# Optimization experiments

Hardware: AMD Instinct MI355X
Metric: run time of the kernel (lower is better)

The kernel has to match this reference:

```python
import jax, jax.numpy as jnp
import numpy as np

N_NODES = 50000
N_EDGES = 800000
D = 256            # node_feat_size
D_EDGE = 16        # edge_feat_size (unused in forward math, as in the original)
G_FEAT = 200       # graph_feat_size
N_TASKS = 1
N_GRAPHS = 512


def _p(key, shape):
    return jax.random.normal(key, shape, dtype=jnp.float32) * 0.05


def setup_inputs() -> dict:
    key = jax.random.key(0)
    ks = jax.random.split(key, 24)
    inp = {
        'node_feats_1': jax.random.normal(ks[0], (N_NODES, D), dtype=jnp.float32),
        'edge_feats_1': jax.random.normal(ks[1], (N_EDGES, D_EDGE), dtype=jnp.float32),
        'node_feats_2': jax.random.normal(ks[2], (N_NODES, D), dtype=jnp.float32),
        'edge_feats_2': jax.random.normal(ks[3], (N_EDGES, D_EDGE), dtype=jnp.float32),
        'src_1': jax.random.randint(ks[4], (N_EDGES,), 0, N_NODES, dtype=jnp.int32),
        'dst_1': jax.random.randint(ks[5], (N_EDGES,), 0, N_NODES, dtype=jnp.int32),
        'graph_ids_1': jnp.sort(jax.random.randint(ks[6], (N_NODES,), 0, N_GRAPHS, dtype=jnp.int32)),
        'src_2': jax.random.randint(ks[7], (N_EDGES,), 0, N_NODES, dtype=jnp.int32),
        'dst_2': jax.random.randint(ks[8], (N_EDGES,), 0, N_NODES, dtype=jnp.int32),
        'graph_ids_2': jnp.sort(jax.random.randint(ks[9], (N_NODES,), 0, N_GRAPHS, dtype=jnp.int32)),
        # GCN layer 1 params (GraphConv weight/bias + residual Linear)
        'W1': _p(ks[10], (D, D)), 'b1': jnp.zeros((D,), jnp.float32),
        'Wr1': _p(ks[11], (D, D)), 'br1': jnp.zeros((D,), jnp.float32),
        # GCN layer 2 params
        'W2': _p(ks[12], (D, D)), 'b2': jnp.zeros((D,), jnp.float32),
        'Wr2': _p(ks[13], (D, D)), 'br2': jnp.zeros((D,), jnp.float32),
        # Readout 1 MLP
        'Ri1': _p(ks[14], (D, D)), 'rbi1': jnp.zeros((D,), jnp.float32),
        'Ro1': _p(ks[15], (D, G_FEAT)), 'rbo1': jnp.zeros((G_FEAT,), jnp.float32),
        # Readout 2 MLP
        'Ri2': _p(ks[16], (D, D)), 'rbi2': jnp.zeros((D,), jnp.float32),
        'Ro2': _p(ks[17], (D, G_FEAT)), 'rbo2': jnp.zeros((G_FEAT,), jnp.float32),
        # Predictor
        'Wp': _p(ks[18], (G_FEAT, N_TASKS)), 'bp': jnp.zeros((N_TASKS,), jnp.float32),
    }
    return inp


def _gcn_layer(h, src, dst, W, b, Wr, br):
    # DGL GraphConv, norm='none': project, aggregate (sum src->dst), bias, relu
    hW = h @ W                                             # [N, D]
    agg = jax.ops.segment_sum(jnp.take(hW, src, axis=0), dst, num_segments=N_NODES)
    conv = jax.nn.relu(agg + b)
    # residual branch: activation(Linear(h))
    res = jax.nn.relu(h @ Wr + br)
    return conv + res                                      # dropout=0, no batchnorm


def _readout(h, graph_ids, Wi, bi, Wo, bo):
    # MLPNodeReadout: Linear -> relu -> Linear, then sum over nodes per graph
    h = jax.nn.relu(h @ Wi + bi)
    h = h @ Wo + bo                                        # [N, G_FEAT]
    return jax.ops.segment_sum(h, graph_ids, num_segments=N_GRAPHS)


def reference(node_feats_1, edge_feats_1, node_feats_2, edge_feats_2,
              src_1, dst_1, graph_ids_1, src_2, dst_2, graph_ids_2,
              W1, b1, Wr1, br1, W2, b2, Wr2, br2,
              Ri1, rbi1, Ro1, rbo1, Ri2, rbi2, Ro2, rbo2, Wp, bp):
    h1 = _gcn_layer(node_feats_1, src_1, dst_1, W1, b1, Wr1, br1)
    g1 = _readout(h1, graph_ids_1, Ri1, rbi1, Ro1, rbo1)
    h2 = _gcn_layer(node_feats_2, src_2, dst_2, W2, b2, Wr2, br2)
    g2 = _readout(h2, graph_ids_2, Ri2, rbi2, Ro2, rbo2)
    g = g1 + g2                                            # [G, G_FEAT]
    return (g @ Wp + bp).reshape(-1)                       # [G * n_tasks]
```

## Files before the change

### kernel.cpp

```cpp
#include <hip/hip_runtime.h>

#define NN 50000
#define NE 800000
#define DD 256
#define GFEAT 200
#define NG 512

typedef __bf16 bf16;
typedef bf16 bf16x4 __attribute__((ext_vector_type(4)));
typedef bf16 bf16x8 __attribute__((ext_vector_type(8)));
typedef float f32x4 __attribute__((ext_vector_type(4)));

__device__ __forceinline__ void gl_lds16(const bf16* g, bf16* l) {
    __builtin_amdgcn_global_load_lds(
        (const __attribute__((address_space(1))) uint32_t*)(g),
        (__attribute__((address_space(3))) uint32_t*)(l), 16, 0, 0);
}

__device__ __forceinline__ bf16x8 frag_ld64(const bf16* s, int R, int C) {
    return *(const bf16x8*)&s[R * 64 + ((C ^ ((R >> 1) & 7)) << 3)];
}

#define EPI_STRIDE 136

__global__ __launch_bounds__(256) void conv_x2_kernel(const float* __restrict__ in0,
                                                      const float* __restrict__ in1,
                                                      bf16* __restrict__ out0,
                                                      bf16* __restrict__ out1, int n4) {
    const float* in = blockIdx.y ? in1 : in0;
    bf16* out = blockIdx.y ? out1 : out0;
    int i = blockIdx.x * 256 + threadIdx.x;
    if (i < n4) {
        float4 v = ((const float4*)in)[i];
        bf16x4 o;
        o[0] = (bf16)v.x; o[1] = (bf16)v.y; o[2] = (bf16)v.z; o[3] = (bf16)v.w;
        ((bf16x4*)out)[i] = o;
    }
}

__global__ __launch_bounds__(256) void conv_w8_kernel(
    const float* __restrict__ w0, const float* __restrict__ w1,
    const float* __restrict__ w2, const float* __restrict__ w3,
    const float* __restrict__ w4, const float* __restrict__ w5,
    const float* __restrict__ w6, const float* __restrict__ w7,
    bf16* __restrict__ out_base) {
    const float* ws[8] = {w0, w1, w2, w3, w4, w5, w6, w7};
    const int Ns[8] = {DD, DD, DD, GFEAT, DD, DD, DD, GFEAT};
    int m = blockIdx.y;
    const float* in = ws[m];
    int N = Ns[m];
    int idx = blockIdx.x * 256 + threadIdx.x;
    int n = idx >> 8, k = idx & 255;
    float v = (n < N) ? in[k * N + n] : 0.f;
    out_base[(size_t)m * 65536 + idx] = (bf16)v;
}

__global__ __launch_bounds__(256) void zero_g_kernel(float* __restrict__ G0,
                                                     float* __restrict__ G1) {
    float* G = blockIdx.y ? G1 : G0;
    int i = blockIdx.x * 256 + threadIdx.x;
    if (i < NG * GFEAT) G[i] = 0.f;
}

#define NBKT   128
#define NPB    391
#define NCHUNK 256
#define CE     ((NE + NCHUNK - 1) / NCHUNK)

__global__ __launch_bounds__(256) void csr_coarse_hist_kernel(
    const int* __restrict__ d0, const int* __restrict__ d1,
    int* __restrict__ cnt0, int* __restrict__ cnt1) {
    const int blk = blockIdx.x, t = threadIdx.x;
    const int* dst = blockIdx.y ? d1 : d0;
    int* cnt = blockIdx.y ? cnt1 : cnt0;
    __shared__ int hist[NBKT];
    if (t < NBKT) hist[t] = 0;
    __syncthreads();
    const int e0 = blk * CE;
    const int e1 = (e0 + CE < NE) ? e0 + CE : NE;
    for (int e = e0 + t; e < e1; e += 256)
        atomicAdd(&hist[dst[e] / NPB], 1);
    __syncthreads();
    if (t < NBKT) cnt[t * NCHUNK + blk] = hist[t];
}

__global__ __launch_bounds__(1024) void csr_scan_kernel(
    int* __restrict__ cnt0, int* __restrict__ cnt1,
    int* __restrict__ offs0, int* __restrict__ offs1) {
    int* cnt = blockIdx.y ? cnt1 : cnt0;
    const int t = threadIdx.x;
    const int PER = (NBKT * NCHUNK) / 1024;
    int v[PER];
    int sum = 0;
    const int base = t * PER;
#pragma unroll
    for (int i = 0; i < PER; i += 4) {
        int4 q = *(const int4*)&cnt[base + i];
        v[i] = q.x; v[i + 1] = q.y; v[i + 2] = q.z; v[i + 3] = q.w;
        sum += q.x + q.y + q.z + q.w;
    }
    __shared__ int s[1024];
    s[t] = sum;
    __syncthreads();
    for (int off = 1; off < 1024; off <<= 1) {
        int a = (t >= off) ? s[t - off] : 0;
        __syncthreads();
        s[t] += a;
        __syncthreads();
    }
    int run = s[t] - sum;
#pragma unroll
    for (int i = 0; i < PER; i++) { int c = v[i]; cnt[base + i] = run; run += c; }
    if (t == 0) (blockIdx.y ? offs1 : offs0)[NN] = NE;
}

__global__ __launch_bounds__(256) void csr_partition_kernel(
    const int* __restrict__ sA, const int* __restrict__ sB,
    const int* __restrict__ d0, const int* __restrict__ d1,
    const int* __restrict__ cnt0, const int* __restrict__ cnt1,
    int2* __restrict__ eb0, int2* __restrict__ eb1) {
    const int blk = blockIdx.x, t = threadIdx.x;
    const int* src = blockIdx.y ? sB : sA;
    const int* dst = blockIdx.y ? d1 : d0;
    const int* cnt = blockIdx.y ? cnt1 : cnt0;
    int2* eb = blockIdx.y ? eb1 : eb0;
    __shared__ int cur[NBKT];
    if (t < NBKT) cur[t] = cnt[t * NCHUNK + blk];
    __syncthreads();
    const int e0 = blk * CE;
    const int e1 = (e0 + CE < NE) ? e0 + CE : NE;
    for (int e = e0 + t; e < e1; e += 256) {
        int d = dst[e], s = src[e];
        int pos = atomicAdd(&cur[d / NPB], 1);
        eb[pos] = make_int2(s, d);
    }
}

__global__ __launch_bounds__(512) void csr_bucket_sort_kernel(
    const int* __restrict__ cnt0, const int* __restrict__ cnt1,
    const int2* __restrict__ eb0, const int2* __restrict__ eb1,
    int* __restrict__ offs0, int* __restrict__ offs1,
    int* __restrict__ csr0, int* __restrict__ csr1) {
    const int b = blockIdx.x, t = threadIdx.x;
    const int* cnt = blockIdx.y ? cnt1 : cnt0;
    const int2* eb = blockIdx.y ? eb1 : eb0;
    int* offs = blockIdx.y ? offs1 : offs0;
    int* csr = blockIdx.y ? csr1 : csr0;
    const int lo = b * NPB;
    const int ncnt = (NN - lo < NPB) ? (NN - lo) : NPB;
    const int beg = cnt[b * NCHUNK];
    const int end = (b == NBKT - 1) ? NE : cnt[(b + 1) * NCHUNK];

    __shared__ int hist[NPB];
    __shared__ int s[512];
    if (t < NPB) hist[t] = 0;
    __syncthreads();
    for (int i = beg + t; i < end; i += 512)
        atomicAdd(&hist[eb[i].y - lo], 1);
    __syncthreads();

    int h = (t < NPB) ? hist[t] : 0;
    s[t] = h;
    __syncthreads();
    for (int off = 1; off < 512; off <<= 1) {
        int a = (t >= off) ? s[t - off] : 0;
        __syncthreads();
        s[t] += a;
        __syncthreads();
    }
    int excl = s[t] - h;
    __syncthreads();
    if (t < NPB) hist[t] = excl;
    if (t < ncnt) offs[lo + t] = beg + excl;
    __syncthreads();

    for (int i = beg + t; i < end; i += 512) {
        int2 v = eb[i];
        int pos = atomicAdd(&hist[v.y - lo], 1);
        csr[beg + pos] = v.x;
    }
}

#define STAGE64(MAT, base_row, CLAMP_M)                                          \
    _Pragma("unroll")                                                            \
    for (int r_ = 0; r_ < 4; r_++) {                                             \
        int flat_ = r_ * 256 + t;                                                \
        int fr_ = flat_ >> 3, fc_ = flat_ & 7;                                   \
        int fcg_ = fc_ ^ ((fr_ >> 1) & 7);                                       \
        int row_ = (base_row) + fr_;                                             \
        if (CLAMP_M && row_ > M - 1) row_ = M - 1;                               \
        gl_lds16(&MAT[(size_t)row_ * 256 + k0 + fcg_ * 8],                       \
                 &(((r_ < 2) ? As : As) )[0] + 0);                               \
    }


__global__ __launch_bounds__(256) void mfma_gemm2_kernel(
    const bf16* __restrict__ A0, const bf16* __restrict__ A1,
    const bf16* __restrict__ Bt0, const bf16* __restrict__ Bt1,
    const float* __restrict__ bias0, const float* __restrict__ bias1,
    bf16* __restrict__ out0, bf16* __restrict__ out1,
    int M, int Nb, int do_relu) {
    const int lid = blockIdx.x;
    const int r8 = lid & 7, cc = (lid >> 3) & 1, g = lid >> 4;
    const int row_blk = g * 8 + r8;
    if (row_blk * 128 >= M) return;
    const bf16* A = blockIdx.y ? A1 : A0;
    const bf16* Bt = blockIdx.y ? Bt1 : Bt0;
    const float* bias = blockIdx.y ? bias1 : bias0;
    bf16* out = blockIdx.y ? out1 : out0;

    __shared__ bf16 smem[16384];
    bf16* As = smem;
    bf16* Bs = smem + 8192;

    const int t    = threadIdx.x;
    const int lane = t & 63;
    const int w    = t >> 6;
    const int row0 = row_blk * 128;
    const int col0 = cc * 128;

    f32x4 acc[4][4] = {};
    const int wm = (w >> 1) * 64, wn = (w & 1) * 64;
    const int fm = lane & 15, fC = lane >> 4;

    for (int k0 = 0; k0 < 256; k0 += 64) {
#pragma unroll
        for (int r = 0; r < 4; r++) {
            int flat = r * 256 + t;
            int fr = flat >> 3, fc = flat & 7;
            int fcg = fc ^ ((fr >> 1) & 7);
            int arow = row0 + fr;
            if (arow > M - 1) arow = M - 1;
            gl_lds16(&A[(size_t)arow * 256 + k0 + fcg * 8], &As[flat * 8]);
        }
#pragma unroll
        for (int r = 0; r < 4; r++) {
            int flat = r * 256 + t;
            int fr = flat >> 3, fc = flat & 7;
            int fcg = fc ^ ((fr >> 1) & 7);
            int brow = col0 + fr;
            gl_lds16(&Bt[(size_t)brow * 256 + k0 + fcg * 8], &Bs[flat * 8]);
        }
        __syncthreads();
#pragma unroll
        for (int s = 0; s < 2; s++) {
            bf16x8 af[4], bfr[4];
#pragma unroll
            for (int i = 0; i < 4; i++) af[i] = frag_ld64(As, wm + i * 16 + fm, s * 4 + fC);
#pragma unroll
            for (int i = 0; i < 4; i++) bfr[i] = frag_ld64(Bs, wn + i * 16 + fm, s * 4 + fC);
#pragma unroll
            for (int i = 0; i < 4; i++)
#pragma unroll
                for (int j = 0; j < 4; j++)
                    acc[i][j] = __builtin_amdgcn_mfma_f32_16x16x32_bf16(af[i], bfr[j], acc[i][j], 0, 0, 0);
        }
        __syncthreads();
    }

    float bv[4];
#pragma unroll
    for (int j = 0; j < 4; j++) {
        int col = col0 + wn + fm + j * 16;
        bv[j] = (col < Nb) ? bias[col] : 0.f;
    }

#pragma unroll
    for (int p = 0; p < 2; p++) {
        if ((w >> 1) == p) {
#pragma unroll
            for (int i = 0; i < 4; i++)
#pragma unroll
                for (int j = 0; j < 4; j++)
#pragma unroll
                    for (int r2 = 0; r2 < 4; r2++) {
                        int rl = i * 16 + (lane >> 4) * 4 + r2;
                        int cl = wn + fm + j * 16;
                        float v = acc[i][j][r2] + bv[j];
                        if (do_relu) v = fmaxf(v, 0.f);
                        smem[rl * EPI_STRIDE + cl] = (bf16)v;
                    }
        }
        __syncthreads();
#pragma unroll
        for (int q = 0; q < 4; q++) {
            int flat = q * 256 + t;
            int rl = flat >> 4, seg = flat & 15;
            int grow = row0 + p * 64 + rl;
            if (grow < M)
                *(bf16x8*)&out[(size_t)grow * 256 + col0 + seg * 8] =
                    *(const bf16x8*)&smem[rl * EPI_STRIDE + seg * 8];
        }
        __syncthreads();
    }
}

__global__ __launch_bounds__(256) void mfma_gemm_fused2_kernel(
    const bf16* __restrict__ A0, const bf16* __restrict__ A1,
    const bf16* __restrict__ Bt2_0, const bf16* __restrict__ Bt2_1,
    const float* __restrict__ bh0, const float* __restrict__ bh1,
    bf16* __restrict__ lo0, bf16* __restrict__ lo1,
    bf16* __restrict__ hi0, bf16* __restrict__ hi1, int M) {
    const int lid = blockIdx.x;
    const int r8 = lid & 7, cc = (lid >> 3) & 3, g = lid >> 5;
    const int row_blk = g * 8 + r8;
    if (row_blk * 128 >= M) return;
    const bf16* A = blockIdx.y ? A1 : A0;
    const bf16* Bt2 = blockIdx.y ? Bt2_1 : Bt2_0;
    const float* bias_hi = blockIdx.y ? bh1 : bh0;
    bf16* out_lo = blockIdx.y ? lo1 : lo0;
    bf16* out_hi = blockIdx.y ? hi1 : hi0;

    __shared__ bf16 smem[16384];
    bf16* As = smem;
    bf16* Bs = smem + 8192;

    const int t    = threadIdx.x;
    const int lane = t & 63;
    const int w    = t >> 6;
    const int row0 = row_blk * 128;
    const int col0 = cc * 128;

    f32x4 acc[4][4] = {};
    const int wm = (w >> 1) * 64, wn = (w & 1) * 64;
    const int fm = lane & 15, fC = lane >> 4;

    for (int k0 = 0; k0 < 256; k0 += 64) {
#pragma unroll
        for (int r = 0; r < 4; r++) {
            int flat = r * 256 + t;
            int fr = flat >> 3, fc = flat & 7;
            int fcg = fc ^ ((fr >> 1) & 7);
            int arow = row0 + fr;
            if (arow > M - 1) arow = M - 1;
            gl_lds16(&A[(size_t)arow * 256 + k0 + fcg * 8], &As[flat * 8]);
        }
#pragma unroll
        for (int r = 0; r < 4; r++) {
            int flat = r * 256 + t;
            int fr = flat >> 3, fc = flat & 7;
            int fcg = fc ^ ((fr >> 1) & 7);
            int brow = col0 + fr;
            gl_lds16(&Bt2[(size_t)brow * 256 + k0 + fcg * 8], &Bs[flat * 8]);
        }
        __syncthreads();
#pragma unroll
        for (int s = 0; s < 2; s++) {
            bf16x8 af[4], bfr[4];
#pragma unroll
            for (int i = 0; i < 4; i++) af[i] = frag_ld64(As, wm + i * 16 + fm, s * 4 + fC);
#pragma unroll
            for (int i = 0; i < 4; i++) bfr[i] = frag_ld64(Bs, wn + i * 16 + fm, s * 4 + fC);
#pragma unroll
            for (int i = 0; i < 4; i++)
#pragma unroll
                for (int j = 0; j < 4; j++)
                    acc[i][j] = __builtin_amdgcn_mfma_f32_16x16x32_bf16(af[i], bfr[j], acc[i][j], 0, 0, 0);
        }
        __syncthreads();
    }

    const bool hi = (col0 >= 256);
    bf16* out = hi ? out_hi : out_lo;
    const int cb = hi ? col0 - 256 : col0;

    float bv[4];
#pragma unroll
    for (int j = 0; j < 4; j++) {
        int col = cb + wn + fm + j * 16;
        bv[j] = hi ? bias_hi[col] : 0.f;
    }

#pragma unroll
    for (int p = 0; p < 2; p++) {
        if ((w >> 1) == p) {
#pragma unroll
            for (int i = 0; i < 4; i++)
#pragma unroll
                for (int j = 0; j < 4; j++)
#pragma unroll
                    for (int r2 = 0; r2 < 4; r2++) {
                        int rl = i * 16 + (lane >> 4) * 4 + r2;
                        int cl = wn + fm + j * 16;
                        float v = acc[i][j][r2] + bv[j];
                        if (hi) v = fmaxf(v, 0.f);
                        smem[rl * EPI_STRIDE + cl] = (bf16)v;
                    }
        }
        __syncthreads();
#pragma unroll
        for (int q = 0; q < 4; q++) {
            int flat = q * 256 + t;
            int rl = flat >> 4, seg = flat & 15;
            int grow = row0 + p * 64 + rl;
            if (grow < M)
                *(bf16x8*)&out[(size_t)grow * 256 + cb + seg * 8] =
                    *(const bf16x8*)&smem[rl * EPI_STRIDE + seg * 8];
        }
        __syncthreads();
    }
}

__global__ __launch_bounds__(256) void mfma_gemm_reduce2_kernel(
    const bf16* __restrict__ A0, const bf16* __restrict__ A1,
    const bf16* __restrict__ Bt0, const bf16* __restrict__ Bt1,
    const float* __restrict__ bias0, const float* __restrict__ bias1,
    const int* __restrict__ gid0, const int* __restrict__ gid1,
    float* __restrict__ G0, float* __restrict__ G1, int M, int Nb) {
    const int lid = blockIdx.x;
    const int r8 = lid & 7, cc = (lid >> 3) & 1, g = lid >> 4;
    const int row_blk = g * 8 + r8;
    if (row_blk * 128 >= M) return;
    const bf16* A = blockIdx.y ? A1 : A0;
    const bf16* Bt = blockIdx.y ? Bt1 : Bt0;
    const float* bias = blockIdx.y ? bias1 : bias0;
    const int* gids = blockIdx.y ? gid1 : gid0;
    float* G = blockIdx.y ? G1 : G0;

    __shared__ bf16 smem[16384];
    bf16* As = smem;
    bf16* Bs = smem + 8192;

    const int t    = threadIdx.x;
    const int lane = t & 63;
    const int w    = t >> 6;
    const int row0 = row_blk * 128;
    const int col0 = cc * 128;

    f32x4 acc[4][4] = {};
    const int wm = (w >> 1) * 64, wn = (w & 1) * 64;
    const int fm = lane & 15, fC = lane >> 4;

    for (int k0 = 0; k0 < 256; k0 += 64) {
#pragma unroll
        for (int r = 0; r < 4; r++) {
            int flat = r * 256 + t;
            int fr = flat >> 3, fc = flat & 7;
            int fcg = fc ^ ((fr >> 1) & 7);
            int arow = row0 + fr;
            if (arow > M - 1) arow = M - 1;
            gl_lds16(&A[(size_t)arow * 256 + k0 + fcg * 8], &As[flat * 8]);
        }
#pragma unroll
        for (int r = 0; r < 4; r++) {
            int flat = r * 256 + t;
            int fr = flat >> 3, fc = flat & 7;
            int fcg = fc ^ ((fr >> 1) & 7);
            int brow = col0 + fr;
            gl_lds16(&Bt[(size_t)brow * 256 + k0 + fcg * 8], &Bs[flat * 8]);
        }
        __syncthreads();
#pragma unroll
        for (int s = 0; s < 2; s++) {
            bf16x8 af[4], bfr[4];
#pragma unroll
            for (int i = 0; i < 4; i++) af[i] = frag_ld64(As, wm + i * 16 + fm, s * 4 + fC);
#pragma unroll
            for (int i = 0; i < 4; i++) bfr[i] = frag_ld64(Bs, wn + i * 16 + fm, s * 4 + fC);
#pragma unroll
            for (int i = 0; i < 4; i++)
#pragma unroll
                for (int j = 0; j < 4; j++)
                    acc[i][j] = __builtin_amdgcn_mfma_f32_16x16x32_bf16(af[i], bfr[j], acc[i][j], 0, 0, 0);
        }
        __syncthreads();
    }

    float bv[4];
#pragma unroll
    for (int j = 0; j < 4; j++) {
        int col = col0 + wn + fm + j * 16;
        bv[j] = (col < Nb) ? bias[col] : 0.f;
    }

#pragma unroll
    for (int p = 0; p < 2; p++) {
        if ((w >> 1) == p) {
#pragma unroll
            for (int i = 0; i < 4; i++)
#pragma unroll
                for (int j = 0; j < 4; j++)
#pragma unroll
                    for (int r2 = 0; r2 < 4; r2++) {
                        int rl = i * 16 + (lane >> 4) * 4 + r2;
                        int cl = wn + fm + j * 16;
                        smem[rl * EPI_STRIDE + cl] = (bf16)(acc[i][j][r2] + bv[j]);
                    }
        }
        __syncthreads();
        {
            int c = t & 127, rh = t >> 7;
            int colg = col0 + c;
            if (colg < Nb) {
                float run = 0.f;
                int gprev = -1;
                for (int r = 0; r < 32; r++) {
                    int grow = row0 + p * 64 + rh * 32 + r;
                    if (grow >= M) break;
                    int gg = gids[grow];
                    if (gg != gprev) {
                        if (gprev >= 0) atomicAdd(&G[(size_t)gprev * GFEAT + colg], run);
                        run = 0.f;
                        gprev = gg;
                    }
                    run += (float)smem[(rh * 32 + r) * EPI_STRIDE + c];
                }
                if (gprev >= 0) atomicAdd(&G[(size_t)gprev * GFEAT + colg], run);
            }
        }
        __syncthreads();
    }
}

__global__ __launch_bounds__(256) void agg_combine2_kernel(
    const bf16* __restrict__ hW0, const bf16* __restrict__ hW1,
    const int* __restrict__ csr0, const int* __restrict__ csr1,
    const int* __restrict__ offs0, const int* __restrict__ offs1,
    const float* __restrict__ bias0, const float* __restrict__ bias1,
    const bf16* __restrict__ res0, const bf16* __restrict__ res1,
    bf16* __restrict__ H0, bf16* __restrict__ H1, int n_nodes) {
    const bf16* hW = blockIdx.y ? hW1 : hW0;
    const int* csr_src = blockIdx.y ? csr1 : csr0;
    const int* offsets = blockIdx.y ? offs1 : offs0;
    const float* bias = blockIdx.y ? bias1 : bias0;
    const bf16* res = blockIdx.y ? res1 : res0;
    bf16* H = blockIdx.y ? H1 : H0;

    int wave = threadIdx.x >> 6;
    int lane = threadIdx.x & 63;
    int node = blockIdx.x * 4 + wave;
    if (node >= n_nodes) return;
    int beg = offsets[node], end = offsets[node + 1];
    const int half = lane >> 5;
    const int fo   = (lane & 31) * 8;

    float acc[8] = {};
    int j = beg;
    for (; j + 6 + half < end; j += 8) {
        int s0 = csr_src[j + half];
        int s1 = csr_src[j + 2 + half];
        int s2 = csr_src[j + 4 + half];
        int s3 = csr_src[j + 6 + half];
        bf16x8 v0 = *(const bf16x8*)&hW[(size_t)s0 * DD + fo];
        bf16x8 v1 = *(const bf16x8*)&hW[(size_t)s1 * DD + fo];
        bf16x8 v2 = *(const bf16x8*)&hW[(size_t)s2 * DD + fo];
        bf16x8 v3 = *(const bf16x8*)&hW[(size_t)s3 * DD + fo];
#pragma unroll
        for (int q = 0; q < 8; q++) acc[q] += (float)v0[q];
#pragma unroll
        for (int q = 0; q < 8; q++) acc[q] += (float)v1[q];
#pragma unroll
        for (int q = 0; q < 8; q++) acc[q] += (float)v2[q];
#pragma unroll
        for (int q = 0; q < 8; q++) acc[q] += (float)v3[q];
    }
    for (; j + half < end; j += 2) {
        int s = csr_src[j + half];
        bf16x8 v = *(const bf16x8*)&hW[(size_t)s * DD + fo];
#pragma unroll
        for (int q = 0; q < 8; q++) acc[q] += (float)v[q];
    }
#pragma unroll
    for (int q = 0; q < 8; q++) acc[q] += __shfl_xor(acc[q], 32, 64);

    if (half == 0) {
        float4 b0 = *(const float4*)&bias[fo];
        float4 b1 = *(const float4*)&bias[fo + 4];
        bf16x8 rv = *(const bf16x8*)&res[(size_t)node * DD + fo];
        bf16x8 o;
        o[0] = (bf16)(fmaxf(acc[0] + b0.x, 0.f) + (float)rv[0]);
        o[1] = (bf16)(fmaxf(acc[1] + b0.y, 0.f) + (float)rv[1]);
        o[2] = (bf16)(fmaxf(acc[2] + b0.z, 0.f) + (float)rv[2]);
        o[3] = (bf16)(fmaxf(acc[3] + b0.w, 0.f) + (float)rv[3]);
        o[4] = (bf16)(fmaxf(acc[4] + b1.x, 0.f) + (float)rv[4]);
        o[5] = (bf16)(fmaxf(acc[5] + b1.y, 0.f) + (float)rv[5]);
        o[6] = (bf16)(fmaxf(acc[6] + b1.z, 0.f) + (float)rv[6]);
        o[7] = (bf16)(fmaxf(acc[7] + b1.w, 0.f) + (float)rv[7]);
        *(bf16x8*)&H[(size_t)node * DD + fo] = o;
    }
}

__global__ __launch_bounds__(256) void predictor_kernel(const float* __restrict__ G1,
                                                        const float* __restrict__ G2,
                                                        const float* __restrict__ Wp,
                                                        const float* __restrict__ bp,
                                                        float* __restrict__ out) {
    int i = blockIdx.x * 256 + threadIdx.x;
    if (i >= NG) return;
    float acc = bp[0];
    for (int f = 0; f < GFEAT; f++)
        acc += (G1[i * GFEAT + f] + G2[i * GFEAT + f]) * Wp[f];
    out[i] = acc;
}

extern "C" void kernel_launch(void* const* d_in, const int* in_sizes, int n_in,
                              void* d_out, int out_size, void* d_ws, size_t ws_size,
                              hipStream_t stream) {
    const float* X1   = (const float*)d_in[0];
    const float* X2   = (const float*)d_in[2];
    const int*   src1 = (const int*)d_in[4];
    const int*   dst1 = (const int*)d_in[5];
    const int*   gid1 = (const int*)d_in[6];
    const int*   src2 = (const int*)d_in[7];
    const int*   dst2 = (const int*)d_in[8];
    const int*   gid2 = (const int*)d_in[9];
    const float* W1  = (const float*)d_in[10]; const float* b1  = (const float*)d_in[11];
    const float* Wr1 = (const float*)d_in[12]; const float* br1 = (const float*)d_in[13];
    const float* W2  = (const float*)d_in[14]; const float* b2  = (const float*)d_in[15];
    const float* Wr2 = (const float*)d_in[16]; const float* br2 = (const float*)d_in[17];
    const float* Ri1 = (const float*)d_in[18]; const float* rbi1 = (const float*)d_in[19];
    const float* Ro1 = (const float*)d_in[20]; const float* rbo1 = (const float*)d_in[21];
    const float* Ri2 = (const float*)d_in[22]; const float* rbi2 = (const float*)d_in[23];
    const float* Ro2 = (const float*)d_in[24]; const float* rbo2 = (const float*)d_in[25];
    const float* Wp  = (const float*)d_in[26]; const float* bp  = (const float*)d_in[27];

    const size_t NB = (size_t)NN * DD * sizeof(bf16);
    char* p = (char*)d_ws;
    bf16* XbH1 = (bf16*)p; p += NB;
    bf16* XbH2 = (bf16*)p; p += NB;
    bf16* hWR1 = (bf16*)p; p += NB;
    bf16* hWR2 = (bf16*)p; p += NB;
    bf16* res1 = (bf16*)p; p += NB;
    bf16* res2 = (bf16*)p; p += NB;
    float* G1  = (float*)p; p += (size_t)NG * GFEAT * sizeof(float);
    float* G2  = (float*)p; p += (size_t)NG * GFEAT * sizeof(float);
    bf16* Wbase = (bf16*)p; p += 8 * 65536 * sizeof(bf16);
    int* offs1 = (int*)p; p += (NN + 1) * sizeof(int);
    int* offs2 = (int*)p; p += (NN + 1) * sizeof(int);
    int* cnt1  = (int*)p; p += NBKT * NCHUNK * sizeof(int);
    int* cnt2  = (int*)p; p += NBKT * NCHUNK * sizeof(int);
    int* csr1  = (int*)p; p += NE * sizeof(int);
    int* csr2  = (int*)p; p += NE * sizeof(int);
    int2* eb1 = (int2*)hWR1;
    int2* eb2 = (int2*)hWR2;

    zero_g_kernel<<<dim3((NG * GFEAT + 255) / 256, 2), 256, 0, stream>>>(G1, G2);
    conv_w8_kernel<<<dim3(256, 8), 256, 0, stream>>>(W1, Wr1, Ri1, Ro1, W2, Wr2, Ri2, Ro2, Wbase);
    conv_x2_kernel<<<dim3((NN * DD / 4 + 255) / 256, 2), 256, 0, stream>>>(
        X1, X2, XbH1, XbH2, NN * DD / 4);

    csr_coarse_hist_kernel<<<dim3(NCHUNK, 2), 256, 0, stream>>>(dst1, dst2, cnt1, cnt2);
    csr_scan_kernel<<<dim3(1, 2), 1024, 0, stream>>>(cnt1, cnt2, offs1, offs2);
    csr_partition_kernel<<<dim3(NCHUNK, 2), 256, 0, stream>>>(
        src1, src2, dst1, dst2, cnt1, cnt2, eb1, eb2);
    csr_bucket_sort_kernel<<<dim3(NBKT, 2), 512, 0, stream>>>(
        cnt1, cnt2, eb1, eb2, offs1, offs2, csr1, csr2);

    mfma_gemm_fused2_kernel<<<dim3(49 * 32, 2), 256, 0, stream>>>(
        XbH1, XbH2, Wbase + 0 * 65536, Wbase + 4 * 65536, br1, br2,
        hWR1, hWR2, res1, res2, NN);
    agg_combine2_kernel<<<dim3((NN + 3) / 4, 2), 256, 0, stream>>>(
        hWR1, hWR2, csr1, csr2, offs1, offs2, b1, b2, res1, res2, XbH1, XbH2, NN);
    mfma_gemm2_kernel<<<dim3(49 * 16, 2), 256, 0, stream>>>(
        XbH1, XbH2, Wbase + 2 * 65536, Wbase + 6 * 65536, rbi1, rbi2,
        hWR1, hWR2, NN, DD, 1);
    mfma_gemm_reduce2_kernel<<<dim3(49 * 16, 2), 256, 0, stream>>>(
        hWR1, hWR2, Wbase + 3 * 65536, Wbase + 7 * 65536, rbo1, rbo2,
        gid1, gid2, G1, G2, NN, GFEAT);

    predictor_kernel<<<(NG + 255) / 256, 256, 0, stream>>>(G1, G2, Wp, bp, (float*)d_out);
}
```

Before: 557.4 us.

## Fuse fp32-to-bf16 input conversion into first GEMM and enlarge GEMM tiles

Removes the standalone fp32-to-bf16 conversion pass over both node feature matrices. The first GEMM now reads fp32 rows directly, converts them in registers, and writes the swizzled bf16 tile into LDS itself. All three GEMM kernels also move from 256-thread, 128-row tiles to 512-thread, 256-row tiles, so each B tile is reused across more rows. In exchange, the A loads in the first GEMM become synchronous register loads instead of direct-to-LDS loads, and the larger tiles use more LDS per block, which may reduce occupancy.

```diff
diff --git a/kernel.cpp b/kernel.cpp
--- a/kernel.cpp
+++ b/kernel.cpp
@@ -22,21 +22,6 @@
 }
 
 #define EPI_STRIDE 136
-
-__global__ __launch_bounds__(256) void conv_x2_kernel(const float* __restrict__ in0,
-                                                      const float* __restrict__ in1,
-                                                      bf16* __restrict__ out0,
-                                                      bf16* __restrict__ out1, int n4) {
-    const float* in = blockIdx.y ? in1 : in0;
-    bf16* out = blockIdx.y ? out1 : out0;
-    int i = blockIdx.x * 256 + threadIdx.x;
-    if (i < n4) {
-        float4 v = ((const float4*)in)[i];
-        bf16x4 o;
-        o[0] = (bf16)v.x; o[1] = (bf16)v.y; o[2] = (bf16)v.z; o[3] = (bf16)v.w;
-        ((bf16x4*)out)[i] = o;
-    }
-}
 
 __global__ __launch_bounds__(256) void conv_w8_kernel(
     const float* __restrict__ w0, const float* __restrict__ w1,
@@ -181,20 +166,8 @@
     }
 }
 
-#define STAGE64(MAT, base_row, CLAMP_M)                                          \
-    _Pragma("unroll")                                                            \
-    for (int r_ = 0; r_ < 4; r_++) {                                             \
-        int flat_ = r_ * 256 + t;                                                \
-        int fr_ = flat_ >> 3, fc_ = flat_ & 7;                                   \
-        int fcg_ = fc_ ^ ((fr_ >> 1) & 7);                                       \
-        int row_ = (base_row) + fr_;                                             \
-        if (CLAMP_M && row_ > M - 1) row_ = M - 1;                               \
-        gl_lds16(&MAT[(size_t)row_ * 256 + k0 + fcg_ * 8],                       \
-                 &(((r_ < 2) ? As : As) )[0] + 0);                               \
-    }
-
-
-__global__ __launch_bounds__(256) void mfma_gemm2_kernel(
+
+__global__ __launch_bounds__(512) void mfma_gemm2_kernel(
     const bf16* __restrict__ A0, const bf16* __restrict__ A1,
     const bf16* __restrict__ Bt0, const bf16* __restrict__ Bt1,
     const float* __restrict__ bias0, const float* __restrict__ bias1,
@@ -203,20 +176,20 @@
     const int lid = blockIdx.x;
     const int r8 = lid & 7, cc = (lid >> 3) & 1, g = lid >> 4;
     const int row_blk = g * 8 + r8;
-    if (row_blk * 128 >= M) return;
+    if (row_blk * 256 >= M) return;
     const bf16* A = blockIdx.y ? A1 : A0;
     const bf16* Bt = blockIdx.y ? Bt1 : Bt0;
     const float* bias = blockIdx.y ? bias1 : bias0;
     bf16* out = blockIdx.y ? out1 : out0;
 
-    __shared__ bf16 smem[16384];
+    __shared__ bf16 smem[24576];
     bf16* As = smem;
-    bf16* Bs = smem + 8192;
+    bf16* Bs = smem + 16384;
 
     const int t    = threadIdx.x;
     const int lane = t & 63;
     const int w    = t >> 6;
-    const int row0 = row_blk * 128;
+    const int row0 = row_blk * 256;
     const int col0 = cc * 128;
 
     f32x4 acc[4][4] = {};
@@ -226,7 +199,7 @@
     for (int k0 = 0; k0 < 256; k0 += 64) {
 #pragma unroll
         for (int r = 0; r < 4; r++) {
-            int flat = r * 256 + t;
+            int flat = r * 512 + t;
             int fr = flat >> 3, fc = flat & 7;
             int fcg = fc ^ ((fr >> 1) & 7);
             int arow = row0 + fr;
@@ -234,8 +207,8 @@
             gl_lds16(&A[(size_t)arow * 256 + k0 + fcg * 8], &As[flat * 8]);
         }
 #pragma unroll
-        for (int r = 0; r < 4; r++) {
-            int flat = r * 256 + t;
+        for (int r = 0; r < 2; r++) {
+            int flat = r * 512 + t;
             int fr = flat >> 3, fc = flat & 7;
             int fcg = fc ^ ((fr >> 1) & 7);
             int brow = col0 + fr;
@@ -266,7 +239,7 @@
     }
 
 #pragma unroll
-    for (int p = 0; p < 2; p++) {
+    for (int p = 0; p < 4; p++) {
         if ((w >> 1) == p) {
 #pragma unroll
             for (int i = 0; i < 4; i++)
@@ -283,8 +256,8 @@
         }
         __syncthreads();
 #pragma unroll
-        for (int q = 0; q < 4; q++) {
-            int flat = q * 256 + t;
+        for (int q = 0; q < 2; q++) {
+            int flat = q * 512 + t;
             int rl = flat >> 4, seg = flat & 15;
             int grow = row0 + p * 64 + rl;
             if (grow < M)
@@ -295,8 +268,8 @@
     }
 }
 
-__global__ __launch_bounds__(256) void mfma_gemm_fused2_kernel(
-    const bf16* __restrict__ A0, const bf16* __restrict__ A1,
+__global__ __launch_bounds__(512) void mfma_gemm_fusedconv2_kernel(
+    const float* __restrict__ X0, const float* __restrict__ X1,
     const bf16* __restrict__ Bt2_0, const bf16* __restrict__ Bt2_1,
     const float* __restrict__ bh0, const float* __restrict__ bh1,
     bf16* __restrict__ lo0, bf16* __restrict__ lo1,
@@ -304,21 +277,21 @@
     const int lid = blockIdx.x;
     const int r8 = lid & 7, cc = (lid >> 3) & 3, g = lid >> 5;
     const int row_blk = g * 8 + r8;
-    if (row_blk * 128 >= M) return;
-    const bf16* A = blockIdx.y ? A1 : A0;
+    if (row_blk * 256 >= M) return;
+    const float* Xf = blockIdx.y ? X1 : X0;
     const bf16* Bt2 = blockIdx.y ? Bt2_1 : Bt2_0;
     const float* bias_hi = blockIdx.y ? bh1 : bh0;
     bf16* out_lo = blockIdx.y ? lo1 : lo0;
     bf16* out_hi = blockIdx.y ? hi1 : hi0;
 
-    __shared__ bf16 smem[16384];
+    __shared__ bf16 smem[24576];
     bf16* As = smem;
-    bf16* Bs = smem + 8192;
+    bf16* Bs = smem + 16384;
 
     const int t    = threadIdx.x;
     const int lane = t & 63;
     const int w    = t >> 6;
-    const int row0 = row_blk * 128;
+    const int row0 = row_blk * 256;
     const int col0 = cc * 128;
 
     f32x4 acc[4][4] = {};
@@ -327,22 +300,27 @@
 
     for (int k0 = 0; k0 < 256; k0 += 64) {
 #pragma unroll
-        for (int r = 0; r < 4; r++) {
-            int flat = r * 256 + t;
-            int fr = flat >> 3, fc = flat & 7;
-            int fcg = fc ^ ((fr >> 1) & 7);
-            int arow = row0 + fr;
-            if (arow > M - 1) arow = M - 1;
-            gl_lds16(&A[(size_t)arow * 256 + k0 + fcg * 8], &As[flat * 8]);
-        }
-#pragma unroll
-        for (int r = 0; r < 4; r++) {
-            int flat = r * 256 + t;
+        for (int r = 0; r < 2; r++) {
+            int flat = r * 512 + t;
             int fr = flat >> 3, fc = flat & 7;
             int fcg = fc ^ ((fr >> 1) & 7);
             int brow = col0 + fr;
             gl_lds16(&Bt2[(size_t)brow * 256 + k0 + fcg * 8], &Bs[flat * 8]);
         }
+#pragma unroll
+        for (int r = 0; r < 4; r++) {
+            int flat = r * 512 + t;
+            int fr = flat >> 3, fc = flat & 7;
+            int arow = row0 + fr;
+            if (arow > M - 1) arow = M - 1;
+            const float* gsrc = &Xf[(size_t)arow * 256 + k0 + fc * 8];
+            float4 u0 = *(const float4*)gsrc;
+            float4 u1 = *(const float4*)(gsrc + 4);
+            bf16x8 o;
+            o[0] = (bf16)u0.x; o[1] = (bf16)u0.y; o[2] = (bf16)u0.z; o[3] = (bf16)u0.w;
+            o[4] = (bf16)u1.x; o[5] = (bf16)u1.y; o[6] = (bf16)u1.z; o[7] = (bf16)u1.w;
+            *(bf16x8*)&As[fr * 64 + (fc ^ ((fr >> 1) & 7)) * 8] = o;
+        }
         __syncthreads();
 #pragma unroll
         for (int s = 0; s < 2; s++) {
@@ -372,7 +350,7 @@
     }
 
 #pragma unroll
-    for (int p = 0; p < 2; p++) {
+    for (int p = 0; p < 4; p++) {
         if ((w >> 1) == p) {
 #pragma unroll
             for (int i = 0; i < 4; i++)
@@ -389,8 +367,8 @@
         }
         __syncthreads();
 #pragma unroll
-        for (int q = 0; q < 4; q++) {
-            int flat = q * 256 + t;
+        for (int q = 0; q < 2; q++) {
+            int flat = q * 512 + t;
             int rl = flat >> 4, seg = flat & 15;
             int grow = row0 + p * 64 + rl;
             if (grow < M)
@@ -401,7 +379,7 @@
     }
 }
 
-__global__ __launch_bounds__(256) void mfma_gemm_reduce2_kernel(
+__global__ __launch_bounds__(512) void mfma_gemm_reduce2_kernel(
     const bf16* __restrict__ A0, const bf16* __restrict__ A1,
     const bf16* __restrict__ Bt0, const bf16* __restrict__ Bt1,
     const float* __restrict__ bias0, const float* __restrict__ bias1,
@@ -410,21 +388,21 @@
     const int lid = blockIdx.x;
     const int r8 = lid & 7, cc = (lid >> 3) & 1, g = lid >> 4;
     const int row_blk = g * 8 + r8;
-    if (row_blk * 128 >= M) return;
+    if (row_blk * 256 >= M) return;
     const bf16* A = blockIdx.y ? A1 : A0;
     const bf16* Bt = blockIdx.y ? Bt1 : Bt0;
     const float* bias = blockIdx.y ? bias1 : bias0;
     const int* gids = blockIdx.y ? gid1 : gid0;
     float* G = blockIdx.y ? G1 : G0;
 
-    __shared__ bf16 smem[16384];
+    __shared__ bf16 smem[24576];
     bf16* As = smem;
-    bf16* Bs = smem + 8192;
+    bf16* Bs = smem + 16384;
 
     const int t    = threadIdx.x;
     const int lane = t & 63;
     const int w    = t >> 6;
-    const int row0 = row_blk * 128;
+    const int row0 = row_blk * 256;
     const int col0 = cc * 128;
 
     f32x4 acc[4][4] = {};
@@ -434,7 +412,7 @@
     for (int k0 = 0; k0 < 256; k0 += 64) {
 #pragma unroll
         for (int r = 0; r < 4; r++) {
-            int flat = r * 256 + t;
+            int flat = r * 512 + t;
             int fr = flat >> 3, fc = flat & 7;
             int fcg = fc ^ ((fr >> 1) & 7);
             int arow = row0 + fr;
@@ -442,8 +420,8 @@
             gl_lds16(&A[(size_t)arow * 256 + k0 + fcg * 8], &As[flat * 8]);
         }
 #pragma unroll
-        for (int r = 0; r < 4; r++) {
-            int flat = r * 256 + t;
+        for (int r = 0; r < 2; r++) {
+            int flat = r * 512 + t;
             int fr = flat >> 3, fc = flat & 7;
             int fcg = fc ^ ((fr >> 1) & 7);
             int brow = col0 + fr;
@@ -474,7 +452,7 @@
     }
 
 #pragma unroll
-    for (int p = 0; p < 2; p++) {
+    for (int p = 0; p < 4; p++) {
         if ((w >> 1) == p) {
 #pragma unroll
             for (int i = 0; i < 4; i++)
@@ -494,8 +472,8 @@
             if (colg < Nb) {
                 float run = 0.f;
                 int gprev = -1;
-                for (int r = 0; r < 32; r++) {
-                    int grow = row0 + p * 64 + rh * 32 + r;
+                for (int r = 0; r < 16; r++) {
+                    int grow = row0 + p * 64 + rh * 16 + r;
                     if (grow >= M) break;
                     int gg = gids[grow];
                     if (gg != gprev) {
@@ -503,7 +481,7 @@
                         run = 0.f;
                         gprev = gg;
                     }
-                    run += (float)smem[(rh * 32 + r) * EPI_STRIDE + c];
+                    run += (float)smem[(rh * 16 + r) * EPI_STRIDE + c];
                 }
                 if (gprev >= 0) atomicAdd(&G[(size_t)gprev * GFEAT + colg], run);
             }
@@ -616,8 +594,8 @@
 
     const size_t NB = (size_t)NN * DD * sizeof(bf16);
     char* p = (char*)d_ws;
-    bf16* XbH1 = (bf16*)p; p += NB;
-    bf16* XbH2 = (bf16*)p; p += NB;
+    bf16* H1   = (bf16*)p; p += NB;
+    bf16* H2   = (bf16*)p; p += NB;
     bf16* hWR1 = (bf16*)p; p += NB;
     bf16* hWR2 = (bf16*)p; p += NB;
     bf16* res1 = (bf16*)p; p += NB;
@@ -636,8 +614,6 @@
 
     zero_g_kernel<<<dim3((NG * GFEAT + 255) / 256, 2), 256, 0, stream>>>(G1, G2);
     conv_w8_kernel<<<dim3(256, 8), 256, 0, stream>>>(W1, Wr1, Ri1, Ro1, W2, Wr2, Ri2, Ro2, Wbase);
-    conv_x2_kernel<<<dim3((NN * DD / 4 + 255) / 256, 2), 256, 0, stream>>>(
-        X1, X2, XbH1, XbH2, NN * DD / 4);
 
     csr_coarse_hist_kernel<<<dim3(NCHUNK, 2), 256, 0, stream>>>(dst1, dst2, cnt1, cnt2);
     csr_scan_kernel<<<dim3(1, 2), 1024, 0, stream>>>(cnt1, cnt2, offs1, offs2);
@@ -646,15 +622,15 @@
     csr_bucket_sort_kernel<<<dim3(NBKT, 2), 512, 0, stream>>>(
         cnt1, cnt2, eb1, eb2, offs1, offs2, csr1, csr2);
 
-    mfma_gemm_fused2_kernel<<<dim3(49 * 32, 2), 256, 0, stream>>>(
-        XbH1, XbH2, Wbase + 0 * 65536, Wbase + 4 * 65536, br1, br2,
+    mfma_gemm_fusedconv2_kernel<<<dim3(25 * 32, 2), 512, 0, stream>>>(
+        X1, X2, Wbase + 0 * 65536, Wbase + 4 * 65536, br1, br2,
         hWR1, hWR2, res1, res2, NN);
     agg_combine2_kernel<<<dim3((NN + 3) / 4, 2), 256, 0, stream>>>(
-        hWR1, hWR2, csr1, csr2, offs1, offs2, b1, b2, res1, res2, XbH1, XbH2, NN);
-    mfma_gemm2_kernel<<<dim3(49 * 16, 2), 256, 0, stream>>>(
-        XbH1, XbH2, Wbase + 2 * 65536, Wbase + 6 * 65536, rbi1, rbi2,
+        hWR1, hWR2, csr1, csr2, offs1, offs2, b1, b2, res1, res2, H1, H2, NN);
+    mfma_gemm2_kernel<<<dim3(25 * 16, 2), 512, 0, stream>>>(
+        H1, H2, Wbase + 2 * 65536, Wbase + 6 * 65536, rbi1, rbi2,
         hWR1, hWR2, NN, DD, 1);
-    mfma_gemm_reduce2_kernel<<<dim3(49 * 16, 2), 256, 0, stream>>>(
+    mfma_gemm_reduce2_kernel<<<dim3(25 * 16, 2), 512, 0, stream>>>(
         hWR1, hWR2, Wbase + 3 * 65536, Wbase + 7 * 65536, rbo1, rbo2,
         gid1, gid2, G1, G2, NN, GFEAT);
 
```

Measured after the change: 544.6 us. 2.3% less time.

## Double-buffer GEMM LDS tiles, fuse fp32-to-bf16 input conversion into first GEMM

Applied to the files above, without the earlier changes.

All three MFMA GEMM kernels now use double-buffered LDS tiles, prefetching the next K slice while the current one feeds the MFMAs, with explicit vmcnt waits in place of full syncthreads. The first GEMM reads fp32 node features directly and converts them to bf16 in registers before writing to LDS, which removes the separate conversion kernel and its bf16 round trip through memory. The weight transpose kernel now goes through an LDS tile so both reads and writes are coalesced. LDS use per block doubles, which may reduce occupancy, and the fused kernel reads fp32 A once per column block, so it fetches more bytes than the old bf16 path.

```diff
diff --git a/kernel.cpp b/kernel.cpp
--- a/kernel.cpp
+++ b/kernel.cpp
@@ -21,24 +21,22 @@
     return *(const bf16x8*)&s[R * 64 + ((C ^ ((R >> 1) & 7)) << 3)];
 }
 
+__device__ __forceinline__ void stage_tile(const bf16* src, bf16* dst,
+                                           int base_row, int maxrow, int k0, int t) {
+#pragma unroll
+    for (int r = 0; r < 4; r++) {
+        int flat = r * 256 + t;
+        int fr = flat >> 3, fc = flat & 7;
+        int fcg = fc ^ ((fr >> 1) & 7);
+        int row = base_row + fr;
+        if (row > maxrow) row = maxrow;
+        gl_lds16(&src[(size_t)row * 256 + k0 + fcg * 8], &dst[flat * 8]);
+    }
+}
+
 #define EPI_STRIDE 136
 
-__global__ __launch_bounds__(256) void conv_x2_kernel(const float* __restrict__ in0,
-                                                      const float* __restrict__ in1,
-                                                      bf16* __restrict__ out0,
-                                                      bf16* __restrict__ out1, int n4) {
-    const float* in = blockIdx.y ? in1 : in0;
-    bf16* out = blockIdx.y ? out1 : out0;
-    int i = blockIdx.x * 256 + threadIdx.x;
-    if (i < n4) {
-        float4 v = ((const float4*)in)[i];
-        bf16x4 o;
-        o[0] = (bf16)v.x; o[1] = (bf16)v.y; o[2] = (bf16)v.z; o[3] = (bf16)v.w;
-        ((bf16x4*)out)[i] = o;
-    }
-}
-
-__global__ __launch_bounds__(256) void conv_w8_kernel(
+__global__ __launch_bounds__(256) void conv_w8t_kernel(
     const float* __restrict__ w0, const float* __restrict__ w1,
     const float* __restrict__ w2, const float* __restrict__ w3,
     const float* __restrict__ w4, const float* __restrict__ w5,
@@ -46,13 +44,25 @@
     bf16* __restrict__ out_base) {
     const float* ws[8] = {w0, w1, w2, w3, w4, w5, w6, w7};
     const int Ns[8] = {DD, DD, DD, GFEAT, DD, DD, DD, GFEAT};
-    int m = blockIdx.y;
+    const int m = blockIdx.x >> 4;
+    const int tile = blockIdx.x & 15;
+    const int k0 = (tile >> 2) * 64, n0 = (tile & 3) * 64;
     const float* in = ws[m];
-    int N = Ns[m];
-    int idx = blockIdx.x * 256 + threadIdx.x;
-    int n = idx >> 8, k = idx & 255;
-    float v = (n < N) ? in[k * N + n] : 0.f;
-    out_base[(size_t)m * 65536 + idx] = (bf16)v;
+    const int N = Ns[m];
+    const int t = threadIdx.x;
+    __shared__ float ts[64][65];
+#pragma unroll
+    for (int r = 0; r < 16; r++) {
+        int dk = r * 4 + (t >> 6), dn = t & 63;
+        int n = n0 + dn;
+        ts[dk][dn] = (n < N) ? in[(k0 + dk) * N + n] : 0.f;
+    }
+    __syncthreads();
+#pragma unroll
+    for (int r = 0; r < 16; r++) {
+        int dn = r * 4 + (t >> 6), dk = t & 63;
+        out_base[(size_t)m * 65536 + (size_t)(n0 + dn) * 256 + k0 + dk] = (bf16)ts[dk][dn];
+    }
 }
 
 __global__ __launch_bounds__(256) void zero_g_kernel(float* __restrict__ G0,
@@ -181,18 +191,6 @@
     }
 }
 
-#define STAGE64(MAT, base_row, CLAMP_M)                                          \
-    _Pragma("unroll")                                                            \
-    for (int r_ = 0; r_ < 4; r_++) {                                             \
-        int flat_ = r_ * 256 + t;                                                \
-        int fr_ = flat_ >> 3, fc_ = flat_ & 7;                                   \
-        int fcg_ = fc_ ^ ((fr_ >> 1) & 7);                                       \
-        int row_ = (base_row) + fr_;                                             \
-        if (CLAMP_M && row_ > M - 1) row_ = M - 1;                               \
-        gl_lds16(&MAT[(size_t)row_ * 256 + k0 + fcg_ * 8],                       \
-                 &(((r_ < 2) ? As : As) )[0] + 0);                               \
-    }
-
 
 __global__ __launch_bounds__(256) void mfma_gemm2_kernel(
     const bf16* __restrict__ A0, const bf16* __restrict__ A1,
@@ -209,9 +207,9 @@
     const float* bias = blockIdx.y ? bias1 : bias0;
     bf16* out = blockIdx.y ? out1 : out0;
 
-    __shared__ bf16 smem[16384];
-    bf16* As = smem;
-    bf16* Bs = smem + 8192;
+    __shared__ bf16 smem[32768];
+    bf16* Asb[2] = {smem, smem + 8192};
+    bf16* Bsb[2] = {smem + 16384, smem + 24576};
 
     const int t    = threadIdx.x;
     const int lane = t & 63;
@@ -223,39 +221,34 @@
     const int wm = (w >> 1) * 64, wn = (w & 1) * 64;
     const int fm = lane & 15, fC = lane >> 4;
 
-    for (int k0 = 0; k0 < 256; k0 += 64) {
-#pragma unroll
-        for (int r = 0; r < 4; r++) {
-            int flat = r * 256 + t;
-            int fr = flat >> 3, fc = flat & 7;
-            int fcg = fc ^ ((fr >> 1) & 7);
-            int arow = row0 + fr;
-            if (arow > M - 1) arow = M - 1;
-            gl_lds16(&A[(size_t)arow * 256 + k0 + fcg * 8], &As[flat * 8]);
-        }
-#pragma unroll
-        for (int r = 0; r < 4; r++) {
-            int flat = r * 256 + t;
-            int fr = flat >> 3, fc = flat & 7;
-            int fcg = fc ^ ((fr >> 1) & 7);
-            int brow = col0 + fr;
-            gl_lds16(&Bt[(size_t)brow * 256 + k0 + fcg * 8], &Bs[flat * 8]);
-        }
-        __syncthreads();
+    stage_tile(A, Asb[0], row0, M - 1, 0, t);
+    stage_tile(Bt, Bsb[0], col0, 255, 0, t);
+#pragma unroll
+    for (int k = 0; k < 4; k++) {
+        if (k < 3) {
+            stage_tile(A, Asb[(k + 1) & 1], row0, M - 1, (k + 1) * 64, t);
+            stage_tile(Bt, Bsb[(k + 1) & 1], col0, 255, (k + 1) * 64, t);
+            asm volatile("s_waitcnt vmcnt(8)" ::: "memory");
+        } else {
+            asm volatile("s_waitcnt vmcnt(0)" ::: "memory");
+        }
+        __builtin_amdgcn_s_barrier();
+        const bf16* cA = Asb[k & 1];
+        const bf16* cB = Bsb[k & 1];
 #pragma unroll
         for (int s = 0; s < 2; s++) {
             bf16x8 af[4], bfr[4];
 #pragma unroll
-            for (int i = 0; i < 4; i++) af[i] = frag_ld64(As, wm + i * 16 + fm, s * 4 + fC);
-#pragma unroll
-            for (int i = 0; i < 4; i++) bfr[i] = frag_ld64(Bs, wn + i * 16 + fm, s * 4 + fC);
+            for (int i = 0; i < 4; i++) af[i] = frag_ld64(cA, wm + i * 16 + fm, s * 4 + fC);
+#pragma unroll
+            for (int i = 0; i < 4; i++) bfr[i] = frag_ld64(cB, wn + i * 16 + fm, s * 4 + fC);
 #pragma unroll
             for (int i = 0; i < 4; i++)
 #pragma unroll
                 for (int j = 0; j < 4; j++)
                     acc[i][j] = __builtin_amdgcn_mfma_f32_16x16x32_bf16(af[i], bfr[j], acc[i][j], 0, 0, 0);
         }
-        __syncthreads();
+        __builtin_amdgcn_s_barrier();
     }
 
     float bv[4];
@@ -295,8 +288,8 @@
     }
 }
 
-__global__ __launch_bounds__(256) void mfma_gemm_fused2_kernel(
-    const bf16* __restrict__ A0, const bf16* __restrict__ A1,
+__global__ __launch_bounds__(256) void mfma_gemm_fusedconv2_kernel(
+    const float* __restrict__ X0, const float* __restrict__ X1,
     const bf16* __restrict__ Bt2_0, const bf16* __restrict__ Bt2_1,
     const float* __restrict__ bh0, const float* __restrict__ bh1,
     bf16* __restrict__ lo0, bf16* __restrict__ lo1,
@@ -305,15 +298,15 @@
     const int r8 = lid & 7, cc = (lid >> 3) & 3, g = lid >> 5;
     const int row_blk = g * 8 + r8;
     if (row_blk * 128 >= M) return;
-    const bf16* A = blockIdx.y ? A1 : A0;
+    const float* Xf = blockIdx.y ? X1 : X0;
     const bf16* Bt2 = blockIdx.y ? Bt2_1 : Bt2_0;
     const float* bias_hi = blockIdx.y ? bh1 : bh0;
     bf16* out_lo = blockIdx.y ? lo1 : lo0;
     bf16* out_hi = blockIdx.y ? hi1 : hi0;
 
-    __shared__ bf16 smem[16384];
-    bf16* As = smem;
-    bf16* Bs = smem + 8192;
+    __shared__ bf16 smem[32768];
+    bf16* Asb[2] = {smem, smem + 8192};
+    bf16* Bsb[2] = {smem + 16384, smem + 24576};
 
     const int t    = threadIdx.x;
     const int lane = t & 63;
@@ -325,39 +318,68 @@
     const int wm = (w >> 1) * 64, wn = (w & 1) * 64;
     const int fm = lane & 15, fC = lane >> 4;
 
-    for (int k0 = 0; k0 < 256; k0 += 64) {
+    float4 ua[4], ub[4];
+    auto loadA = [&](int k0) {
 #pragma unroll
         for (int r = 0; r < 4; r++) {
             int flat = r * 256 + t;
             int fr = flat >> 3, fc = flat & 7;
-            int fcg = fc ^ ((fr >> 1) & 7);
             int arow = row0 + fr;
             if (arow > M - 1) arow = M - 1;
-            gl_lds16(&A[(size_t)arow * 256 + k0 + fcg * 8], &As[flat * 8]);
-        }
+            const float* gsrc = &Xf[(size_t)arow * 256 + k0 + fc * 8];
+            ua[r] = *(const float4*)gsrc;
+            ub[r] = *(const float4*)(gsrc + 4);
+        }
+    };
+    auto writeA = [&](bf16* dstA) {
 #pragma unroll
         for (int r = 0; r < 4; r++) {
             int flat = r * 256 + t;
             int fr = flat >> 3, fc = flat & 7;
-            int fcg = fc ^ ((fr >> 1) & 7);
-            int brow = col0 + fr;
-            gl_lds16(&Bt2[(size_t)brow * 256 + k0 + fcg * 8], &Bs[flat * 8]);
-        }
-        __syncthreads();
+            bf16x8 o;
+            o[0] = (bf16)ua[r].x; o[1] = (bf16)ua[r].y; o[2] = (bf16)ua[r].z; o[3] = (bf16)ua[r].w;
+            o[4] = (bf16)ub[r].x; o[5] = (bf16)ub[r].y; o[6] = (bf16)ub[r].z; o[7] = (bf16)ub[r].w;
+            *(bf16x8*)&dstA[fr * 64 + ((fc ^ ((fr >> 1) & 7)) << 3)] = o;
+        }
+    };
+
+    loadA(0);
+    stage_tile(Bt2, Bsb[0], col0, 511, 0, t);
+    asm volatile("s_waitcnt vmcnt(4)" ::: "memory");
+    writeA(Asb[0]);
+    asm volatile("s_waitcnt lgkmcnt(0)" ::: "memory");
+
+#pragma unroll
+    for (int k = 0; k < 4; k++) {
+        if (k < 3) {
+            loadA((k + 1) * 64);
+            stage_tile(Bt2, Bsb[(k + 1) & 1], col0, 511, (k + 1) * 64, t);
+            asm volatile("s_waitcnt vmcnt(12)" ::: "memory");
+        } else {
+            asm volatile("s_waitcnt vmcnt(0)" ::: "memory");
+        }
+        __builtin_amdgcn_s_barrier();
+        const bf16* cA = Asb[k & 1];
+        const bf16* cB = Bsb[k & 1];
 #pragma unroll
         for (int s = 0; s < 2; s++) {
             bf16x8 af[4], bfr[4];
 #pragma unroll
-            for (int i = 0; i < 4; i++) af[i] = frag_ld64(As, wm + i * 16 + fm, s * 4 + fC);
-#pragma unroll
-            for (int i = 0; i < 4; i++) bfr[i] = frag_ld64(Bs, wn + i * 16 + fm, s * 4 + fC);
+            for (int i = 0; i < 4; i++) af[i] = frag_ld64(cA, wm + i * 16 + fm, s * 4 + fC);
+#pragma unroll
+            for (int i = 0; i < 4; i++) bfr[i] = frag_ld64(cB, wn + i * 16 + fm, s * 4 + fC);
 #pragma unroll
             for (int i = 0; i < 4; i++)
 #pragma unroll
                 for (int j = 0; j < 4; j++)
                     acc[i][j] = __builtin_amdgcn_mfma_f32_16x16x32_bf16(af[i], bfr[j], acc[i][j], 0, 0, 0);
         }
-        __syncthreads();
+        if (k < 3) {
+            asm volatile("s_waitcnt vmcnt(4)" ::: "memory");
+            writeA(Asb[(k + 1) & 1]);
+            asm volatile("s_waitcnt lgkmcnt(0)" ::: "memory");
+        }
+        __builtin_amdgcn_s_barrier();
     }
 
     const bool hi = (col0 >= 256);
@@ -417,9 +439,9 @@
     const int* gids = blockIdx.y ? gid1 : gid0;
     float* G = blockIdx.y ? G1 : G0;
 
-    __shared__ bf16 smem[16384];
-    bf16* As = smem;
-    bf16* Bs = smem + 8192;
+    __shared__ bf16 smem[32768];
+    bf16* Asb[2] = {smem, smem + 8192};
+    bf16* Bsb[2] = {smem + 16384, smem + 24576};
 
     const int t    = threadIdx.x;
     const int lane = t & 63;
@@ -431,39 +453,34 @@
     const int wm = (w >> 1) * 64, wn = (w & 1) * 64;
     const int fm = lane & 15, fC = lane >> 4;
 
-    for (int k0 = 0; k0 < 256; k0 += 64) {
-#pragma unroll
-        for (int r = 0; r < 4; r++) {
-            int flat = r * 256 + t;
-            int fr = flat >> 3, fc = flat & 7;
-            int fcg = fc ^ ((fr >> 1) & 7);
-            int arow = row0 + fr;
-            if (arow > M - 1) arow = M - 1;
-            gl_lds16(&A[(size_t)arow * 256 + k0 + fcg * 8], &As[flat * 8]);
-        }
-#pragma unroll
-        for (int r = 0; r < 4; r++) {
-            int flat = r * 256 + t;
-            int fr = flat >> 3, fc = flat & 7;
-            int fcg = fc ^ ((fr >> 1) & 7);
-            int brow = col0 + fr;
-            gl_lds16(&Bt[(size_t)brow * 256 + k0 + fcg * 8], &Bs[flat * 8]);
-        }
-        __syncthreads();
+    stage_tile(A, Asb[0], row0, M - 1, 0, t);
+    stage_tile(Bt, Bsb[0], col0, 255, 0, t);
+#pragma unroll
+    for (int k = 0; k < 4; k++) {
+        if (k < 3) {
+            stage_tile(A, Asb[(k + 1) & 1], row0, M - 1, (k + 1) * 64, t);
+            stage_tile(Bt, Bsb[(k + 1) & 1], col0, 255, (k + 1) * 64, t);
+            asm volatile("s_waitcnt vmcnt(8)" ::: "memory");
+        } else {
+            asm volatile("s_waitcnt vmcnt(0)" ::: "memory");
+        }
+        __builtin_amdgcn_s_barrier();
+        const bf16* cA = Asb[k & 1];
+        const bf16* cB = Bsb[k & 1];
 #pragma unroll
         for (int s = 0; s < 2; s++) {
             bf16x8 af[4], bfr[4];
 #pragma unroll
-            for (int i = 0; i < 4; i++) af[i] = frag_ld64(As, wm + i * 16 + fm, s * 4 + fC);
-#pragma unroll
-            for (int i = 0; i < 4; i++) bfr[i] = frag_ld64(Bs, wn + i * 16 + fm, s * 4 + fC);
+            for (int i = 0; i < 4; i++) af[i] = frag_ld64(cA, wm + i * 16 + fm, s * 4 + fC);
+#pragma unroll
+            for (int i = 0; i < 4; i++) bfr[i] = frag_ld64(cB, wn + i * 16 + fm, s * 4 + fC);
 #pragma unroll
             for (int i = 0; i < 4; i++)
 #pragma unroll
                 for (int j = 0; j < 4; j++)
                     acc[i][j] = __builtin_amdgcn_mfma_f32_16x16x32_bf16(af[i], bfr[j], acc[i][j], 0, 0, 0);
         }
-        __syncthreads();
+        __builtin_amdgcn_s_barrier();
     }
 
     float bv[4];
@@ -616,8 +633,8 @@
 
     const size_t NB = (size_t)NN * DD * sizeof(bf16);
     char* p = (char*)d_ws;
-    bf16* XbH1 = (bf16*)p; p += NB;
-    bf16* XbH2 = (bf16*)p; p += NB;
+    bf16* H1   = (bf16*)p; p += NB;
+    bf16* H2   = (bf16*)p; p += NB;
     bf16* hWR1 = (bf16*)p; p += NB;
     bf16* hWR2 = (bf16*)p; p += NB;
     bf16* res1 = (bf16*)p; p += NB;
@@ -635,9 +652,7 @@
     int2* eb2 = (int2*)hWR2;
 
     zero_g_kernel<<<dim3((NG * GFEAT + 255) / 256, 2), 256, 0, stream>>>(G1, G2);
-    conv_w8_kernel<<<dim3(256, 8), 256, 0, stream>>>(W1, Wr1, Ri1, Ro1, W2, Wr2, Ri2, Ro2, Wbase);
-    conv_x2_kernel<<<dim3((NN * DD / 4 + 255) / 256, 2), 256, 0, stream>>>(
-        X1, X2, XbH1, XbH2, NN * DD / 4);
+    conv_w8t_kernel<<<128, 256, 0, stream>>>(W1, Wr1, Ri1, Ro1, W2, Wr2, Ri2, Ro2, Wbase);
 
     csr_coarse_hist_kernel<<<dim3(NCHUNK, 2), 256, 0, stream>>>(dst1, dst2, cnt1, cnt2);
     csr_scan_kernel<<<dim3(1, 2), 1024, 0, stream>>>(cnt1, cnt2, offs1, offs2);
@@ -646,13 +661,13 @@
     csr_bucket_sort_kernel<<<dim3(NBKT, 2), 512, 0, stream>>>(
         cnt1, cnt2, eb1, eb2, offs1, offs2, csr1, csr2);
 
-    mfma_gemm_fused2_kernel<<<dim3(49 * 32, 2), 256, 0, stream>>>(
-        XbH1, XbH2, Wbase + 0 * 65536, Wbase + 4 * 65536, br1, br2,
+    mfma_gemm_fusedconv2_kernel<<<dim3(49 * 32, 2), 256, 0, stream>>>(
+        X1, X2, Wbase + 0 * 65536, Wbase + 4 * 65536, br1, br2,
         hWR1, hWR2, res1, res2, NN);
     agg_combine2_kernel<<<dim3((NN + 3) / 4, 2), 256, 0, stream>>>(
-        hWR1, hWR2, csr1, csr2, offs1, offs2, b1, b2, res1, res2, XbH1, XbH2, NN);
+        hWR1, hWR2, csr1, csr2, offs1, offs2, b1, b2, res1, res2, H1, H2, NN);
     mfma_gemm2_kernel<<<dim3(49 * 16, 2), 256, 0, stream>>>(
-        XbH1, XbH2, Wbase + 2 * 65536, Wbase + 6 * 65536, rbi1, rbi2,
+        H1, H2, Wbase + 2 * 65536, Wbase + 6 * 65536, rbi1, rbi2,
         hWR1, hWR2, NN, DD, 1);
     mfma_gemm_reduce2_kernel<<<dim3(49 * 16, 2), 256, 0, stream>>>(
         hWR1, hWR2, Wbase + 3 * 65536, Wbase + 7 * 65536, rbo1, rbo2,
```

Measured after the change: 556.6 us. Within noise of the previous version (-0.1%).
